# Kernel tuning notes

Measured on AMD Instinct MI355X. Metric: run time of the kernel, lower is better.

## Reference

```python
import jax, jax.numpy as jnp
import numpy as np

INV_SCALE = 1.0 / (0.5 * 9)  # module's inv_scale_factor; qk is DIVIDED by this (i.e. * 4.5)


def setup_inputs() -> dict:
    key0 = jax.random.key(0)
    ks = jax.random.split(key0, 8)
    B, Sq, Sk, D, Dv = 8, 2048, 2048, 128, 256
    return {
        "query": jax.random.normal(ks[0], (B, Sq, D), dtype=jnp.float32),
        "key": jax.random.normal(ks[1], (B, Sk, D), dtype=jnp.float32),
        "value": jax.random.normal(ks[2], (B, Sk, Dv), dtype=jnp.float32),
        "mask": jax.random.normal(ks[3], (B, Sq, Sk), dtype=jnp.float32),
        # Linear weights stored torch-style as [out_features, in_features]
        "W0": jax.random.normal(ks[4], (D, D), dtype=jnp.float32) * (1.0 / np.sqrt(D)),
        "W1": jax.random.normal(ks[5], (D, D), dtype=jnp.float32) * (1.0 / np.sqrt(D)),
        "W2": jax.random.normal(ks[6], (D, Dv), dtype=jnp.float32) * (1.0 / np.sqrt(Dv)),
        "Wout": jax.random.normal(ks[7], (Dv, D), dtype=jnp.float32) * (1.0 / np.sqrt(D)),
    }


def reference(query, key, value, mask, W0, W1, W2, Wout):
    r1 = jnp.einsum("bqd,od->bqo", query, W0)          # [B,Sq,128]
    r2 = jnp.einsum("bkd,od->bko", key, W1)            # [B,Sk,128]
    r3 = jnp.einsum("bkv,ov->bko", value, W2)          # [B,Sk,128]
    qk = jnp.einsum("bqd,bkd->bqk", r1, r2)            # [B,Sq,Sk]
    scaled_qk = qk / INV_SCALE
    softmax_qk = jax.nn.softmax(scaled_qk, axis=-1)
    # dropout is identity in eval mode (deterministic reference)
    v1 = jnp.einsum("bqk,bko->bqo", softmax_qk, r3)    # [B,Sq,128]
    v2 = jnp.einsum("bqo,vo->bqv", v1, Wout)           # [B,Sq,256]
    output = v2 + jnp.einsum("bqk,bkv->bqv", mask, value)
    return output
```

## Files before the change

### kernel.cpp

```cpp
#include <hip/hip_runtime.h>
#include <cstdint>

typedef __attribute__((ext_vector_type(8))) __bf16 bf16x8;
typedef __attribute__((ext_vector_type(4))) __bf16 bf16x4;
typedef __attribute__((ext_vector_type(4))) float f32x4;

#define MFMA16(a, b, c) __builtin_amdgcn_mfma_f32_16x16x32_bf16((a), (b), (c), 0, 0, 0)
#define WAITV(N) asm volatile("s_waitcnt vmcnt(" #N ")" ::: "memory")

static constexpr int SEQ = 2048;
static constexpr int DV = 256;
static constexpr float QK_SCALE = 4.5f;

__device__ __forceinline__ bf16x4 cvt4(float4 v) {
    bf16x4 y;
    y[0] = (__bf16)v.x; y[1] = (__bf16)v.y; y[2] = (__bf16)v.z; y[3] = (__bf16)v.w;
    return y;
}

__device__ __forceinline__ void gl_lds16(const void* g, void* l) {
    __builtin_amdgcn_global_load_lds((const __attribute__((address_space(1))) uint32_t*)g,
                                     (__attribute__((address_space(3))) uint32_t*)l, 16, 0, 0);
}

template <int K, int TRANS>
__device__ __forceinline__ void proj_body(const float* __restrict__ X,
                                          const float* __restrict__ W,
                                          __bf16* __restrict__ out,
                                          float outScale, int m0, char* smem) {
    auto ldsX = (__bf16(*)[136])smem;
    auto ldsW = (__bf16(*)[136])(smem + 64 * 136 * 2);

    const int t = threadIdx.x;
    const int w = t >> 6, l = t & 63, lrow = l & 15, lq = l >> 4;

    f32x4 acc[8];
#pragma unroll
    for (int i = 0; i < 8; ++i) acc[i] = f32x4{0.f, 0.f, 0.f, 0.f};

#pragma unroll
    for (int kh = 0; kh < K / 128; ++kh) {
        if (kh) __syncthreads();
#pragma unroll
        for (int i = 0; i < 8; ++i) {
            int idx = t + i * 256;
            int r = idx >> 5, c4 = idx & 31;
            float4 v = *(const float4*)(X + (size_t)(m0 + r) * K + kh * 128 + c4 * 4);
            *(bf16x4*)&ldsX[r][c4 * 4] = cvt4(v);
        }
#pragma unroll
        for (int i = 0; i < 16; ++i) {
            int idx = t + i * 256;
            int r = idx >> 5, c4 = idx & 31;
            float4 v = *(const float4*)(W + (size_t)r * K + kh * 128 + c4 * 4);
            *(bf16x4*)&ldsW[r][c4 * 4] = cvt4(v);
        }
        __syncthreads();

        bf16x8 aA[4];
#pragma unroll
        for (int kc = 0; kc < 4; ++kc)
            aA[kc] = *(const bf16x8*)((const char*)&ldsX[w * 16 + lrow][0] + kc * 64 + lq * 16);
#pragma unroll
        for (int nt = 0; nt < 8; ++nt) {
#pragma unroll
            for (int kc = 0; kc < 4; ++kc) {
                bf16x8 bB = *(const bf16x8*)((const char*)&ldsW[nt * 16 + lrow][0] + kc * 64 + lq * 16);
                acc[nt] = MFMA16(aA[kc], bB, acc[nt]);
            }
        }
    }

#pragma unroll
    for (int nt = 0; nt < 8; ++nt) {
        if (TRANS) {
            int gm = m0 + w * 16 + lq * 4;
            int b = gm >> 11, s = gm & 2047;
            int col = nt * 16 + lrow;
            int kt = s >> 5, s32 = s & 31;
            int slot = (s32 >> 3) ^ ((col >> 1) & 3);
            bf16x4 y;
#pragma unroll
            for (int j = 0; j < 4; ++j) y[j] = (__bf16)(acc[nt][j] * outScale);
            *(bf16x4*)(out + (((size_t)b * 64 + kt) * 128 + col) * 32 + slot * 8 + (s32 & 7)) = y;
        } else {
#pragma unroll
            for (int j = 0; j < 4; ++j) {
                int gm = m0 + w * 16 + lq * 4 + j;
                int col = nt * 16 + lrow;
                out[(size_t)gm * 128 + col] = (__bf16)(acc[nt][j] * outScale);
            }
        }
    }
}

__device__ __forceinline__ void vt_body(const float* __restrict__ V,
                                        __bf16* __restrict__ vt, int wg, char* smem) {
    auto tile = (__bf16(*)[72])smem;
    const int t = threadIdx.x;
    const int b = wg >> 7, by = (wg >> 5) & 3, bxx = wg & 31;
    const int s0 = bxx * 64, v0 = by * 64;
#pragma unroll
    for (int i = 0; i < 4; ++i) {
        int idx = t + i * 256;
        int r = idx >> 4, c4 = idx & 15;
        float4 x = *(const float4*)(V + ((size_t)b * SEQ + s0 + r) * DV + v0 + c4 * 4);
        *(bf16x4*)&tile[r][c4 * 4] = cvt4(x);
    }
    __syncthreads();
#pragma unroll
    for (int i = 0; i < 4; ++i) {
        int idx = t + i * 256;
        int vv = idx >> 4, c4 = idx & 15;
        bf16x4 y;
        y[0] = tile[c4 * 4 + 0][vv]; y[1] = tile[c4 * 4 + 1][vv];
        y[2] = tile[c4 * 4 + 2][vv]; y[3] = tile[c4 * 4 + 3][vv];
        int v = v0 + vv;
        int kt = (s0 >> 5) + (c4 >> 3);
        int slot = ((c4 >> 1) & 3) ^ ((v >> 1) & 3);
        *(bf16x4*)(vt + (((size_t)b * 64 + kt) * 256 + v) * 32 + slot * 8 + (c4 & 1) * 4) = y;
    }
}

__global__ __launch_bounds__(256) void k_pre(const float* __restrict__ q,
                                             const float* __restrict__ k,
                                             const float* __restrict__ v,
                                             const float* __restrict__ W0,
                                             const float* __restrict__ W1,
                                             const float* __restrict__ W2,
                                             const float* __restrict__ Wout,
                                             const float* __restrict__ mask,
                                             __bf16* __restrict__ r1s,
                                             __bf16* __restrict__ r2b,
                                             __bf16* __restrict__ r3t,
                                             __bf16* __restrict__ vtb,
                                             __bf16* __restrict__ wob,
                                             __bf16* __restrict__ maskb) {
    __shared__ __align__(16) char smem[52224];
    const int bx = blockIdx.x;
    if (bx < 256) {
        proj_body<128, 0>(q, W0, r1s, QK_SCALE, bx * 64, smem);
    } else if (bx < 512) {
        proj_body<128, 0>(k, W1, r2b, 1.0f, (bx - 256) * 64, smem);
    } else if (bx < 768) {
        proj_body<256, 1>(v, W2, r3t, 1.0f, (bx - 512) * 64, smem);
    } else if (bx < 1792) {
        vt_body(v, vtb, bx - 768, smem);
    } else if (bx < 1824) {
        int i = (bx - 1792) * 256 + threadIdx.x;
        if (i < 8192) {
            float4 x = *(const float4*)(Wout + (size_t)i * 4);
            *(bf16x4*)(wob + (size_t)i * 4) = cvt4(x);
        }
    } else {
        const size_t N = (size_t)8 * 2048 * 2048;
        const size_t stride = (size_t)1024 * 256 * 8;
        size_t i = ((size_t)(bx - 1824) * 256 + threadIdx.x) * 8;
        for (; i < N; i += stride) {
            float4 a = *(const float4*)(mask + i);
            float4 b2 = *(const float4*)(mask + i + 4);
            bf16x8 o;
            o[0] = (__bf16)a.x; o[1] = (__bf16)a.y; o[2] = (__bf16)a.z; o[3] = (__bf16)a.w;
            o[4] = (__bf16)b2.x; o[5] = (__bf16)b2.y; o[6] = (__bf16)b2.z; o[7] = (__bf16)b2.w;
            *(bf16x8*)(maskb + i) = o;
        }
    }
}

__global__ __launch_bounds__(256) void k_flash(const __bf16* __restrict__ r1s,
                                               const __bf16* __restrict__ r2,
                                               const __bf16* __restrict__ r3p,
                                               __bf16* __restrict__ v1p,
                                               float* __restrict__ ml) {
    __shared__ __align__(16) __bf16 r2s[4][32 * 128];
    __shared__ __align__(16) __bf16 r3s[4][128 * 32];
    __shared__ __bf16 plds[4][16][48];

    const int t = threadIdx.x;
    const int bx = (int)((blockIdx.x & 7) * 64 + (blockIdx.x >> 3));
    const int b = bx >> 6, rem = bx & 63, q0 = (rem >> 1) * 64, kh = rem & 1;
    const int w = t >> 6, l = t & 63, lrow = l & 15, lq = l >> 4;

    const __bf16* r1b = r1s + (size_t)b * SEQ * 128;
    const __bf16* r2b = r2 + (size_t)b * SEQ * 128 + (size_t)kh * 1024 * 128;
    const __bf16* r3b = r3p + (size_t)b * 64 * 128 * 32 + (size_t)kh * 32 * 128 * 32;

    bf16x8 aQ[4];
    {
        const __bf16* p = r1b + (size_t)(q0 + w * 16 + lrow) * 128 + lq * 8;
#pragma unroll
        for (int kc = 0; kc < 4; ++kc) aQ[kc] = *(const bf16x8*)(p + kc * 32);
    }

    const __bf16* p_r2[2];
    const __bf16* p_r3[2];
#pragma unroll
    for (int q1 = 0; q1 < 2; ++q1) {
        int r = 8 * w + 4 * q1 + (l >> 4);
        int c = (l & 15) ^ (r & 15);
        p_r2[q1] = r2b + (size_t)r * 128 + c * 8;
        p_r3[q1] = r3b + (size_t)(2 * w + q1) * 512 + l * 8;
    }

    auto stage = [&](int bi) {
#pragma unroll
        for (int q1 = 0; q1 < 2; ++q1) {
            gl_lds16(p_r2[q1], &r2s[bi][(2 * w + q1) * 512]);
            gl_lds16(p_r3[q1], &r3s[bi][(2 * w + q1) * 512]);
            p_r2[q1] += 32 * 128;
            p_r3[q1] += 128 * 32;
        }
    };

    f32x4 acc[8];
#pragma unroll
    for (int i = 0; i < 8; ++i) acc[i] = f32x4{0.f, 0.f, 0.f, 0.f};
    float mrow[4] = {-INFINITY, -INFINITY, -INFINITY, -INFINITY};
    float lsum[4] = {0.f, 0.f, 0.f, 0.f};

    stage(0); stage(1); stage(2);
    for (int it = 0; it < 32; ++it) {
        if (it < 30) { WAITV(8); } else if (it == 30) { WAITV(4); } else { WAITV(0); }
        __builtin_amdgcn_s_barrier();
        __builtin_amdgcn_sched_barrier(0);
        if (it + 3 < 32) stage((it + 3) & 3);
        __builtin_amdgcn_sched_barrier(0);
        const __bf16* R2 = &r2s[it & 3][0];
        const __bf16* R3 = &r3s[it & 3][0];

        f32x4 sc[2];
#pragma unroll
        for (int ct = 0; ct < 2; ++ct) {
            f32x4 s = f32x4{0.f, 0.f, 0.f, 0.f};
#pragma unroll
            for (int kc = 0; kc < 4; ++kc) {
                int p = (kc * 4 + lq) ^ lrow;
                bf16x8 bb = *(const bf16x8*)&R2[(ct * 16 + lrow) * 128 + p * 8];
                s = MFMA16(aQ[kc], bb, s);
            }
            sc[ct] = s;
        }

        float pm[4], al[4];
#pragma unroll
        for (int j = 0; j < 4; ++j) pm[j] = fmaxf(sc[0][j], sc[1][j]);
#pragma unroll
        for (int off = 1; off <= 8; off <<= 1)
#pragma unroll
            for (int j = 0; j < 4; ++j) pm[j] = fmaxf(pm[j], __shfl_xor(pm[j], off, 64));
#pragma unroll
        for (int j = 0; j < 4; ++j) {
            float mn = fmaxf(mrow[j], pm[j]);
            al[j] = __expf(mrow[j] - mn);
            mrow[j] = mn;
        }
        float pr[2][4];
#pragma unroll
        for (int ct = 0; ct < 2; ++ct)
#pragma unroll
            for (int j = 0; j < 4; ++j)
                pr[ct][j] = __expf(sc[ct][j] - mrow[j]);
#pragma unroll
        for (int j = 0; j < 4; ++j)
            lsum[j] = lsum[j] * al[j] + pr[0][j] + pr[1][j];
#pragma unroll
        for (int ot = 0; ot < 8; ++ot)
#pragma unroll
            for (int j = 0; j < 4; ++j) acc[ot][j] *= al[j];

#pragma unroll
        for (int ct = 0; ct < 2; ++ct)
#pragma unroll
            for (int j = 0; j < 4; ++j)
                plds[w][lq * 4 + j][ct * 16 + lrow] = (__bf16)pr[ct][j];
        __builtin_amdgcn_s_waitcnt(0xc07f);
        bf16x8 pA = *(const bf16x8*)&plds[w][lrow][lq * 8];

#pragma unroll
        for (int ot = 0; ot < 8; ++ot) {
            int p = lq ^ ((lrow >> 1) & 3);
            bf16x8 bb = *(const bf16x8*)&R3[(ot * 16 + lrow) * 32 + p * 8];
            acc[ot] = MFMA16(pA, bb, acc[ot]);
        }
    }

#pragma unroll
    for (int off = 1; off <= 8; off <<= 1)
#pragma unroll
        for (int j = 0; j < 4; ++j) lsum[j] += __shfl_xor(lsum[j], off, 64);

    __bf16* vp = v1p + (size_t)kh * 8 * SEQ * 128;
#pragma unroll
    for (int ot = 0; ot < 8; ++ot)
#pragma unroll
        for (int j = 0; j < 4; ++j) {
            int q = q0 + w * 16 + lq * 4 + j;
            float v = acc[ot][j] / lsum[j];
            vp[((size_t)b * SEQ + q) * 128 + ot * 16 + lrow] = (__bf16)v;
        }
    if (lrow == 0) {
#pragma unroll
        for (int j = 0; j < 4; ++j) {
            size_t row = (size_t)b * SEQ + q0 + w * 16 + lq * 4 + j;
            ml[((size_t)kh * 8 * SEQ + row) * 2 + 0] = mrow[j];
            ml[((size_t)kh * 8 * SEQ + row) * 2 + 1] = lsum[j];
        }
    }
}

__global__ __launch_bounds__(512, 4) void k_out(const __bf16* __restrict__ maskb,
                                                const __bf16* __restrict__ vtp,
                                                const __bf16* __restrict__ v1p,
                                                const float* __restrict__ ml,
                                                const __bf16* __restrict__ wob,
                                                float* __restrict__ out) {
    __shared__ __align__(16) __bf16 vbuf[4][256 * 32];
    __shared__ __align__(16) __bf16 mbuf[4][32 * 64];

    const int t = threadIdx.x;
    const int bid = (int)((blockIdx.x & 7) * 64 + (blockIdx.x >> 3));
    const int m0 = bid * 32;
    const int b = m0 >> 11, q0 = m0 & 2047;
    const int w = t >> 6, l = t & 63, lrow = l & 15, lq = l >> 4;
    const int rg = w & 1, cg = w >> 1;

    f32x4 acc[4];
#pragma unroll
    for (int i = 0; i < 4; ++i) acc[i] = f32x4{0.f, 0.f, 0.f, 0.f};

    const __bf16* vsrc[4];
    const __bf16* msrc = nullptr;
    if (w < 4) {
#pragma unroll
        for (int i = 0; i < 4; ++i)
            vsrc[i] = vtp + (size_t)b * 64 * 8192 + (w * 4 + i) * 512 + l * 8;
    } else {
        const int m = w - 4;
        int r = 8 * m + (l >> 3);
        int c = (l & 7) ^ (l >> 3);
        msrc = maskb + ((size_t)(b * 2048 + q0 + r)) * 2048 + c * 8;
    }

    if (w < 4) {
#pragma unroll
        for (int kt = 0; kt < 3; ++kt)
#pragma unroll
            for (int i = 0; i < 4; ++i)
                gl_lds16(vsrc[i] + (size_t)kt * 8192, &vbuf[kt][(w * 4 + i) * 512]);
    } else {
        const int m = w - 4;
#pragma unroll
        for (int e = 0; e < 2; ++e)
            gl_lds16(msrc + (size_t)e * 64, &mbuf[e][m * 512]);
    }

    for (int it = 0; it < 64; ++it) {
        if (w >= 4) {
            const int m = w - 4;
            if ((it & 1) == 0) {
                int en = (it >> 1) + 2;
                if (en <= 31) gl_lds16(msrc + (size_t)en * 64, &mbuf[en & 3][m * 512]);
                if (it <= 58) { WAITV(2); } else if (it == 60) { WAITV(1); } else { WAITV(0); }
            }
        } else {
            if (it <= 61) { WAITV(8); } else if (it == 62) { WAITV(4); } else { WAITV(0); }
        }
        __builtin_amdgcn_s_barrier();
        __builtin_amdgcn_sched_barrier(0);
        if (w < 4 && it + 3 < 64) {
            int kt = it + 3;
#pragma unroll
            for (int i = 0; i < 4; ++i)
                gl_lds16(vsrc[i] + (size_t)kt * 8192, &vbuf[kt & 3][(w * 4 + i) * 512]);
        }
        __builtin_amdgcn_sched_barrier(0);

        const __bf16* Mb = &mbuf[(it >> 1) & 3][0];
        const __bf16* V = &vbuf[it & 3][0];
        const int h = it & 1;
        bf16x8 aM = *(const bf16x8*)&Mb[(rg * 16 + lrow) * 64 + (((h * 4 + lq) ^ (lrow & 7)) * 8)];

        const int pv = lq ^ ((lrow >> 1) & 3);
#pragma unroll
        for (int vt8 = 0; vt8 < 4; ++vt8) {
            bf16x8 bb = *(const bf16x8*)&V[(cg * 64 + vt8 * 16 + lrow) * 32 + pv * 8];
            acc[vt8] = MFMA16(aM, bb, acc[vt8]);
        }
    }

    const int NROW = 8 * SEQ;
    const int row = m0 + rg * 16 + lrow;
    float am0 = ml[(size_t)row * 2 + 0], al0 = ml[(size_t)row * 2 + 1];
    float am1 = ml[((size_t)NROW + row) * 2 + 0], al1 = ml[((size_t)NROW + row) * 2 + 1];
    float M = fmaxf(am0, am1);
    float w0 = al0 * __expf(am0 - M), w1 = al1 * __expf(am1 - M);
    float inv = 1.f / (w0 + w1);
    w0 *= inv; w1 *= inv;
    bf16x8 aV[4];
#pragma unroll
    for (int oc = 0; oc < 4; ++oc) {
        bf16x8 a = *(const bf16x8*)(v1p + (size_t)row * 128 + oc * 32 + lq * 8);
        bf16x8 bh = *(const bf16x8*)(v1p + ((size_t)NROW + row) * 128 + oc * 32 + lq * 8);
        bf16x8 o;
#pragma unroll
        for (int j = 0; j < 8; ++j) o[j] = (__bf16)((float)a[j] * w0 + (float)bh[j] * w1);
        aV[oc] = o;
    }
#pragma unroll
    for (int vt8 = 0; vt8 < 4; ++vt8) {
#pragma unroll
        for (int oc = 0; oc < 4; ++oc) {
            bf16x8 bb = *(const bf16x8*)(wob + (size_t)(cg * 64 + vt8 * 16 + lrow) * 128 + oc * 32 + lq * 8);
            acc[vt8] = MFMA16(aV[oc], bb, acc[vt8]);
        }
    }

#pragma unroll
    for (int vt8 = 0; vt8 < 4; ++vt8)
#pragma unroll
        for (int j = 0; j < 4; ++j) {
            int gq = m0 + rg * 16 + lq * 4 + j;
            out[(size_t)gq * 256 + cg * 64 + vt8 * 16 + lrow] = acc[vt8][j];
        }
}

extern "C" void kernel_launch(void* const* d_in, const int* in_sizes, int n_in,
                              void* d_out, int out_size, void* d_ws, size_t ws_size,
                              hipStream_t stream) {
    const float* q    = (const float*)d_in[0];
    const float* k    = (const float*)d_in[1];
    const float* v    = (const float*)d_in[2];
    const float* mask = (const float*)d_in[3];
    const float* W0   = (const float*)d_in[4];
    const float* W1   = (const float*)d_in[5];
    const float* W2   = (const float*)d_in[6];
    const float* Wout = (const float*)d_in[7];
    float* out = (float*)d_out;

    char* ws = (char*)d_ws;
    __bf16* r1s = (__bf16*)(ws);
    __bf16* r2b = (__bf16*)(ws + (4ull << 20));
    __bf16* r3t = (__bf16*)(ws + (8ull << 20));
    __bf16* vtb = (__bf16*)(ws + (12ull << 20));
    __bf16* wob = (__bf16*)(ws + (20ull << 20));
    __bf16* v1p = (__bf16*)(ws + (25ull << 20));
    float*  mlb = (float*)(ws + (33ull << 20));
    __bf16* mkb = (__bf16*)(ws + (34ull << 20));

    k_pre<<<2848, 256, 0, stream>>>(q, k, v, W0, W1, W2, Wout, mask,
                                    r1s, r2b, r3t, vtb, wob, mkb);
    k_flash<<<512, 256, 0, stream>>>(r1s, r2b, r3t, v1p, mlb);
    k_out<<<512, 512, 0, stream>>>(mkb, vtb, v1p, mlb, wob, out);
}
```

Measured before the change: 339.5 us.

## Split flash attention keys four ways and enlarge output tiles to 64 rows

The flash kernel now splits each batch's key range into four partitions instead of two. It launches twice as many blocks with a double-buffered LDS pipeline and an added end-of-iteration barrier. The output kernel now processes 64 query rows per block with 8 waves covering 128 columns each, so each staged value tile is reused across twice as many mask rows. It merges four partial softmax results instead of two. The aim is more parallelism in attention and less redundant value-tile traffic in the mask GEMM, at the cost of more partial-result traffic and shallower prefetch.

```diff
diff --git a/kernel.cpp b/kernel.cpp
--- a/kernel.cpp
+++ b/kernel.cpp
@@ -172,18 +172,18 @@
                                                const __bf16* __restrict__ r3p,
                                                __bf16* __restrict__ v1p,
                                                float* __restrict__ ml) {
-    __shared__ __align__(16) __bf16 r2s[4][32 * 128];
-    __shared__ __align__(16) __bf16 r3s[4][128 * 32];
+    __shared__ __align__(16) __bf16 r2s[2][32 * 128];
+    __shared__ __align__(16) __bf16 r3s[2][128 * 32];
     __shared__ __bf16 plds[4][16][48];
 
     const int t = threadIdx.x;
-    const int bx = (int)((blockIdx.x & 7) * 64 + (blockIdx.x >> 3));
-    const int b = bx >> 6, rem = bx & 63, q0 = (rem >> 1) * 64, kh = rem & 1;
+    const int bx = (int)((blockIdx.x & 7) * 128 + (blockIdx.x >> 3));
+    const int b = bx >> 7, rem = bx & 127, q0 = (rem >> 2) * 64, kh = rem & 3;
     const int w = t >> 6, l = t & 63, lrow = l & 15, lq = l >> 4;
 
     const __bf16* r1b = r1s + (size_t)b * SEQ * 128;
-    const __bf16* r2b = r2 + (size_t)b * SEQ * 128 + (size_t)kh * 1024 * 128;
-    const __bf16* r3b = r3p + (size_t)b * 64 * 128 * 32 + (size_t)kh * 32 * 128 * 32;
+    const __bf16* r2b = r2 + (size_t)b * SEQ * 128 + (size_t)kh * 512 * 128;
+    const __bf16* r3b = r3p + (size_t)b * 64 * 128 * 32 + (size_t)kh * 16 * 128 * 32;
 
     bf16x8 aQ[4];
     {
@@ -218,15 +218,14 @@
     float mrow[4] = {-INFINITY, -INFINITY, -INFINITY, -INFINITY};
     float lsum[4] = {0.f, 0.f, 0.f, 0.f};
 
-    stage(0); stage(1); stage(2);
-    for (int it = 0; it < 32; ++it) {
-        if (it < 30) { WAITV(8); } else if (it == 30) { WAITV(4); } else { WAITV(0); }
+    stage(0);
+    for (int it = 0; it < 16; ++it) {
+        if (it + 1 < 16) stage((it + 1) & 1);
+        if (it < 15) { WAITV(4); } else { WAITV(0); }
         __builtin_amdgcn_s_barrier();
         __builtin_amdgcn_sched_barrier(0);
-        if (it + 3 < 32) stage((it + 3) & 3);
-        __builtin_amdgcn_sched_barrier(0);
-        const __bf16* R2 = &r2s[it & 3][0];
-        const __bf16* R3 = &r3s[it & 3][0];
+        const __bf16* R2 = &r2s[it & 1][0];
+        const __bf16* R3 = &r3s[it & 1][0];
 
         f32x4 sc[2];
 #pragma unroll
@@ -282,6 +281,7 @@
             bf16x8 bb = *(const bf16x8*)&R3[(ot * 16 + lrow) * 32 + p * 8];
             acc[ot] = MFMA16(pA, bb, acc[ot]);
         }
+        __builtin_amdgcn_s_barrier();
     }
 
 #pragma unroll
@@ -308,42 +308,43 @@
     }
 }
 
-__global__ __launch_bounds__(512, 4) void k_out(const __bf16* __restrict__ maskb,
+__global__ __launch_bounds__(512, 2) void k_out(const __bf16* __restrict__ maskb,
                                                 const __bf16* __restrict__ vtp,
                                                 const __bf16* __restrict__ v1p,
                                                 const float* __restrict__ ml,
                                                 const __bf16* __restrict__ wob,
                                                 float* __restrict__ out) {
-    __shared__ __align__(16) __bf16 vbuf[4][256 * 32];
-    __shared__ __align__(16) __bf16 mbuf[4][32 * 64];
+    __shared__ __align__(16) __bf16 vbuf[3][256 * 32];
+    __shared__ __align__(16) __bf16 mbuf[4][64 * 64];
 
     const int t = threadIdx.x;
-    const int bid = (int)((blockIdx.x & 7) * 64 + (blockIdx.x >> 3));
-    const int m0 = bid * 32;
+    const int bid = (int)((blockIdx.x & 7) * 32 + (blockIdx.x >> 3));
+    const int m0 = bid * 64;
     const int b = m0 >> 11, q0 = m0 & 2047;
     const int w = t >> 6, l = t & 63, lrow = l & 15, lq = l >> 4;
-    const int rg = w & 1, cg = w >> 1;
-
-    f32x4 acc[4];
-#pragma unroll
-    for (int i = 0; i < 4; ++i) acc[i] = f32x4{0.f, 0.f, 0.f, 0.f};
+    const int rg = w & 3, ch = w >> 2;
+
+    f32x4 acc[8];
+#pragma unroll
+    for (int i = 0; i < 8; ++i) acc[i] = f32x4{0.f, 0.f, 0.f, 0.f};
 
     const __bf16* vsrc[4];
-    const __bf16* msrc = nullptr;
+    const __bf16* msrc[2];
     if (w < 4) {
 #pragma unroll
         for (int i = 0; i < 4; ++i)
             vsrc[i] = vtp + (size_t)b * 64 * 8192 + (w * 4 + i) * 512 + l * 8;
     } else {
         const int m = w - 4;
-        int r = 8 * m + (l >> 3);
         int c = (l & 7) ^ (l >> 3);
-        msrc = maskb + ((size_t)(b * 2048 + q0 + r)) * 2048 + c * 8;
+#pragma unroll
+        for (int s = 0; s < 2; ++s)
+            msrc[s] = maskb + ((size_t)(b * 2048 + q0 + 16 * m + 8 * s + (l >> 3))) * 2048 + c * 8;
     }
 
     if (w < 4) {
 #pragma unroll
-        for (int kt = 0; kt < 3; ++kt)
+        for (int kt = 0; kt < 2; ++kt)
 #pragma unroll
             for (int i = 0; i < 4; ++i)
                 gl_lds16(vsrc[i] + (size_t)kt * 8192, &vbuf[kt][(w * 4 + i) * 512]);
@@ -351,7 +352,9 @@
         const int m = w - 4;
 #pragma unroll
         for (int e = 0; e < 2; ++e)
-            gl_lds16(msrc + (size_t)e * 64, &mbuf[e][m * 512]);
+#pragma unroll
+            for (int s = 0; s < 2; ++s)
+                gl_lds16(msrc[s] + (size_t)e * 64, &mbuf[e][(16 * m + 8 * s) * 64]);
     }
 
     for (int it = 0; it < 64; ++it) {
@@ -359,68 +362,85 @@
             const int m = w - 4;
             if ((it & 1) == 0) {
                 int en = (it >> 1) + 2;
-                if (en <= 31) gl_lds16(msrc + (size_t)en * 64, &mbuf[en & 3][m * 512]);
-                if (it <= 58) { WAITV(2); } else if (it == 60) { WAITV(1); } else { WAITV(0); }
+                if (en <= 31) {
+                    gl_lds16(msrc[0] + (size_t)en * 64, &mbuf[en & 3][(16 * m) * 64]);
+                    gl_lds16(msrc[1] + (size_t)en * 64, &mbuf[en & 3][(16 * m + 8) * 64]);
+                }
+                if (it <= 58) { WAITV(4); } else if (it == 60) { WAITV(2); } else { WAITV(0); }
             }
         } else {
-            if (it <= 61) { WAITV(8); } else if (it == 62) { WAITV(4); } else { WAITV(0); }
+            if (it < 63) { WAITV(4); } else { WAITV(0); }
         }
         __builtin_amdgcn_s_barrier();
         __builtin_amdgcn_sched_barrier(0);
-        if (w < 4 && it + 3 < 64) {
-            int kt = it + 3;
+        if (w < 4 && it + 2 < 64) {
+            int kt = it + 2;
 #pragma unroll
             for (int i = 0; i < 4; ++i)
-                gl_lds16(vsrc[i] + (size_t)kt * 8192, &vbuf[kt & 3][(w * 4 + i) * 512]);
+                gl_lds16(vsrc[i] + (size_t)kt * 8192, &vbuf[kt % 3][(w * 4 + i) * 512]);
         }
         __builtin_amdgcn_sched_barrier(0);
 
         const __bf16* Mb = &mbuf[(it >> 1) & 3][0];
-        const __bf16* V = &vbuf[it & 3][0];
+        const __bf16* V = &vbuf[it % 3][0];
         const int h = it & 1;
         bf16x8 aM = *(const bf16x8*)&Mb[(rg * 16 + lrow) * 64 + (((h * 4 + lq) ^ (lrow & 7)) * 8)];
 
         const int pv = lq ^ ((lrow >> 1) & 3);
 #pragma unroll
-        for (int vt8 = 0; vt8 < 4; ++vt8) {
-            bf16x8 bb = *(const bf16x8*)&V[(cg * 64 + vt8 * 16 + lrow) * 32 + pv * 8];
+        for (int vt8 = 0; vt8 < 8; ++vt8) {
+            bf16x8 bb = *(const bf16x8*)&V[(ch * 128 + vt8 * 16 + lrow) * 32 + pv * 8];
             acc[vt8] = MFMA16(aM, bb, acc[vt8]);
         }
     }
 
     const int NROW = 8 * SEQ;
     const int row = m0 + rg * 16 + lrow;
-    float am0 = ml[(size_t)row * 2 + 0], al0 = ml[(size_t)row * 2 + 1];
-    float am1 = ml[((size_t)NROW + row) * 2 + 0], al1 = ml[((size_t)NROW + row) * 2 + 1];
-    float M = fmaxf(am0, am1);
-    float w0 = al0 * __expf(am0 - M), w1 = al1 * __expf(am1 - M);
-    float inv = 1.f / (w0 + w1);
-    w0 *= inv; w1 *= inv;
+    float mp[4], lp[4];
+    float mm = -INFINITY;
+#pragma unroll
+    for (int p = 0; p < 4; ++p) {
+        mp[p] = ml[((size_t)p * NROW + row) * 2 + 0];
+        lp[p] = ml[((size_t)p * NROW + row) * 2 + 1];
+        mm = fmaxf(mm, mp[p]);
+    }
+    float wp[4], wsum = 0.f;
+#pragma unroll
+    for (int p = 0; p < 4; ++p) { wp[p] = lp[p] * __expf(mp[p] - mm); wsum += wp[p]; }
+    float inv = 1.f / wsum;
+#pragma unroll
+    for (int p = 0; p < 4; ++p) wp[p] *= inv;
+
     bf16x8 aV[4];
 #pragma unroll
     for (int oc = 0; oc < 4; ++oc) {
-        bf16x8 a = *(const bf16x8*)(v1p + (size_t)row * 128 + oc * 32 + lq * 8);
-        bf16x8 bh = *(const bf16x8*)(v1p + ((size_t)NROW + row) * 128 + oc * 32 + lq * 8);
-        bf16x8 o;
-#pragma unroll
-        for (int j = 0; j < 8; ++j) o[j] = (__bf16)((float)a[j] * w0 + (float)bh[j] * w1);
-        aV[oc] = o;
-    }
-#pragma unroll
-    for (int vt8 = 0; vt8 < 4; ++vt8) {
+        float s[8];
+#pragma unroll
+        for (int j = 0; j < 8; ++j) s[j] = 0.f;
+#pragma unroll
+        for (int p = 0; p < 4; ++p) {
+            bf16x8 x = *(const bf16x8*)(v1p + ((size_t)p * NROW + row) * 128 + oc * 32 + lq * 8);
+#pragma unroll
+            for (int j = 0; j < 8; ++j) s[j] += wp[p] * (float)x[j];
+        }
+#pragma unroll
+        for (int j = 0; j < 8; ++j) aV[oc][j] = (__bf16)s[j];
+    }
+#pragma unroll
+    for (int vt8 = 0; vt8 < 8; ++vt8) {
 #pragma unroll
         for (int oc = 0; oc < 4; ++oc) {
-            bf16x8 bb = *(const bf16x8*)(wob + (size_t)(cg * 64 + vt8 * 16 + lrow) * 128 + oc * 32 + lq * 8);
+            bf16x8 bb = *(const bf16x8*)(wob + (size_t)(ch * 128 + vt8 * 16 + lrow) * 128 + oc * 32 + lq * 8);
             acc[vt8] = MFMA16(aV[oc], bb, acc[vt8]);
         }
     }
 
 #pragma unroll
-    for (int vt8 = 0; vt8 < 4; ++vt8)
+    for (int vt8 = 0; vt8 < 8; ++vt8)
 #pragma unroll
         for (int j = 0; j < 4; ++j) {
             int gq = m0 + rg * 16 + lq * 4 + j;
-            out[(size_t)gq * 256 + cg * 64 + vt8 * 16 + lrow] = acc[vt8][j];
+            out[(size_t)gq * 256 + ch * 128 + vt8 * 16 + lrow] = acc[vt8][j];
         }
 }
 
@@ -443,12 +463,12 @@
     __bf16* r3t = (__bf16*)(ws + (8ull << 20));
     __bf16* vtb = (__bf16*)(ws + (12ull << 20));
     __bf16* wob = (__bf16*)(ws + (20ull << 20));
-    __bf16* v1p = (__bf16*)(ws + (25ull << 20));
-    float*  mlb = (float*)(ws + (33ull << 20));
-    __bf16* mkb = (__bf16*)(ws + (34ull << 20));
+    float*  mlb = (float*)(ws + (20ull << 20) + (512ull << 10));
+    __bf16* v1p = (__bf16*)(ws + (21ull << 20));
+    __bf16* mkb = (__bf16*)(ws + (37ull << 20));
 
     k_pre<<<2848, 256, 0, stream>>>(q, k, v, W0, W1, W2, Wout, mask,
                                     r1s, r2b, r3t, vtb, wob, mkb);
-    k_flash<<<512, 256, 0, stream>>>(r1s, r2b, r3t, v1p, mlb);
-    k_out<<<512, 512, 0, stream>>>(mkb, vtb, v1p, mlb, wob, out);
-}
+    k_flash<<<1024, 256, 0, stream>>>(r1s, r2b, r3t, v1p, mlb);
+    k_out<<<256, 512, 0, stream>>>(mkb, vtb, v1p, mlb, wob, out);
+}
```

Result: no change. 345.2 us (+1.7%).
